# Kernel tuning notes

Hardware: AMD Instinct MI355X
Metric: run time of the kernel (lower is better)

## Reference

```python
import jax, jax.numpy as jnp
import numpy as np

B, IN_CH, D, H, W = 2, 4, 8, 224, 224
DS = 4
DIM, HEADS, HEAD_DIM, LAYERS = 256, 8, 32, 4
INNER = HEADS * HEAD_DIM
MLP = 4 * DIM
WS = (4, 8, 8)
SHIFT = (2, 4, 4)
WVOL = WS[0] * WS[1] * WS[2]
Hp, Wp = H // DS, W // DS
NW = (D // WS[0]) * (Hp // WS[1]) * (Wp // WS[2])
NBIAS = (2 * WS[0] - 1) * (2 * WS[1] - 1) * (2 * WS[2] - 1)


def _rel_index():
    c = np.stack(np.meshgrid(np.arange(WS[0]), np.arange(WS[1]), np.arange(WS[2]), indexing='ij')).reshape(3, -1)
    r = (c[:, :, None] - c[:, None, :]).transpose(1, 2, 0)
    r[..., 0] += WS[0] - 1
    r[..., 1] += WS[1] - 1
    r[..., 2] += WS[2] - 1
    return r[..., 0] * (2 * WS[1] - 1) * (2 * WS[2] - 1) + r[..., 1] * (2 * WS[2] - 1) + r[..., 2]

REL_IDX = jnp.asarray(_rel_index())  # (WVOL, WVOL)


def _shift_mask():
    # standard Swin shifted-window attention mask on the post-merge grid
    img = np.zeros((D, Hp, Wp), np.int32)
    cnt = 0
    sl = lambda w, s: (slice(0, -w), slice(-w, -s), slice(-s, None))
    for sd in sl(WS[0], SHIFT[0]):
        for sh in sl(WS[1], SHIFT[1]):
            for sw in sl(WS[2], SHIFT[2]):
                img[sd, sh, sw] = cnt
                cnt += 1
    m = img.reshape(D // WS[0], WS[0], Hp // WS[1], WS[1], Wp // WS[2], WS[2])
    m = m.transpose(0, 2, 4, 1, 3, 5).reshape(NW, WVOL)
    return jnp.asarray(np.where(m[:, None, :] != m[:, :, None], -1e9, 0.0).astype(np.float32))

ATTN_MASK = _shift_mask()  # (NW, WVOL, WVOL)


def layer_norm(x, s, b):
    mu = x.mean(-1, keepdims=True)
    var = x.var(-1, keepdims=True)
    return (x - mu) / jnp.sqrt(var + 1e-5) * s + b


def window_attention(x, qkv_w, out_w, out_b, bias_tab, shifted):
    # x: (B, D, Hp, Wp, C) channel-last
    if shifted:
        x = jnp.roll(x, (-SHIFT[0], -SHIFT[1], -SHIFT[2]), axis=(1, 2, 3))
    xw = x.reshape(B, D // WS[0], WS[0], Hp // WS[1], WS[1], Wp // WS[2], WS[2], DIM)
    xw = xw.transpose(0, 1, 3, 5, 2, 4, 6, 7).reshape(B, NW, WVOL, DIM)
    qkv = xw @ qkv_w  # (B, NW, WVOL, 3*INNER)
    q, k, v = jnp.split(qkv, 3, axis=-1)
    split = lambda t: t.reshape(B, NW, WVOL, HEADS, HEAD_DIM).transpose(0, 1, 3, 2, 4)
    q = split(q) * (HEAD_DIM ** -0.5)
    k, v = split(k), split(v)
    attn = jnp.einsum('bwhid,bwhjd->bwhij', q, k)  # (B, NW, H, WVOL, WVOL)
    bias = bias_tab[REL_IDX].transpose(2, 0, 1)  # (H, WVOL, WVOL)
    attn = attn + bias
    if shifted:
        attn = attn + ATTN_MASK[None, :, None]
    attn = jax.nn.softmax(attn, axis=-1)
    o = jnp.einsum('bwhij,bwhjd->bwhid', attn, v)
    o = o.transpose(0, 1, 3, 2, 4).reshape(B, NW, WVOL, INNER)
    o = o @ out_w + out_b
    o = o.reshape(B, D // WS[0], Hp // WS[1], Wp // WS[2], WS[0], WS[1], WS[2], DIM)
    o = o.transpose(0, 1, 4, 2, 5, 3, 6, 7).reshape(B, D, Hp, Wp, DIM)
    if shifted:
        o = jnp.roll(o, SHIFT, axis=(1, 2, 3))
    return o


def setup_inputs() -> dict:
    key = jax.random.key(0)
    ks = jax.random.split(key, 12)
    s = 0.02
    return {
        'x': jax.random.normal(ks[0], (B, IN_CH, D, H, W), jnp.float32),
        'conv_w': jax.random.normal(ks[1], (DIM, IN_CH, 1, DS, DS), jnp.float32) * s,
        'conv_b': jnp.zeros((DIM,), jnp.float32),
        'ln1_s': jnp.ones((LAYERS, DIM), jnp.float32),
        'ln1_b': jnp.zeros((LAYERS, DIM), jnp.float32),
        'qkv_w': jax.random.normal(ks[2], (LAYERS, DIM, 3 * INNER), jnp.float32) * s,
        'out_w': jax.random.normal(ks[3], (LAYERS, INNER, DIM), jnp.float32) * s,
        'out_b': jnp.zeros((LAYERS, DIM), jnp.float32),
        'bias_tab': jax.random.normal(ks[4], (LAYERS, NBIAS, HEADS), jnp.float32) * s,
        'ln2_s': jnp.ones((LAYERS, DIM), jnp.float32),
        'ln2_b': jnp.zeros((LAYERS, DIM), jnp.float32),
        'fc1_w': jax.random.normal(ks[5], (LAYERS, DIM, MLP), jnp.float32) * s,
        'fc1_b': jnp.zeros((LAYERS, MLP), jnp.float32),
        'fc2_w': jax.random.normal(ks[6], (LAYERS, MLP, DIM), jnp.float32) * s,
        'fc2_b': jnp.zeros((LAYERS, DIM), jnp.float32),
    }


def reference(x, conv_w, conv_b, ln1_s, ln1_b, qkv_w, out_w, out_b, bias_tab, ln2_s, ln2_b, fc1_w, fc1_b, fc2_w, fc2_b):
    # patch merge: Conv3d kernel (1, DS, DS) stride (1, DS, DS)
    y = jax.lax.conv_general_dilated(
        x, conv_w, window_strides=(1, DS, DS), padding='VALID',
        dimension_numbers=('NCDHW', 'OIDHW', 'NCDHW'))
    y = y + conv_b[None, :, None, None, None]
    y = y.transpose(0, 2, 3, 4, 1)  # (B, D, Hp, Wp, DIM) channel-last
    for i in range(LAYERS):
        shifted = (i % 2 == 1)
        y = y + window_attention(layer_norm(y, ln1_s[i], ln1_b[i]),
                                 qkv_w[i], out_w[i], out_b[i], bias_tab[i], shifted)
        h = layer_norm(y, ln2_s[i], ln2_b[i])
        h = jax.nn.gelu(h @ fc1_w[i] + fc1_b[i]) @ fc2_w[i] + fc2_b[i]
        y = y + h
    return y.transpose(0, 4, 1, 2, 3)  # (B, DIM, D, Hp, Wp)
```

## Files before the change

kernel.cpp:

```cpp
#include <hip/hip_runtime.h>

typedef unsigned short ushort_t;
typedef unsigned int   uint_t;

#define NTOK 50176
#define NWIN 98
#define NBIAS 1575

typedef __attribute__((ext_vector_type(8))) short bf16x8;
typedef __attribute__((ext_vector_type(4))) float floatx4;

static __device__ __forceinline__ ushort_t f2b(float f) {
    union { float f; uint_t u; } v; v.f = f;
    uint_t u = v.u + 0x7fffu + ((v.u >> 16) & 1u);
    return (ushort_t)(u >> 16);
}

__global__ void transpose_w(const float* __restrict__ src, ushort_t* __restrict__ dst,
                            int K, int N) {
    long base = (long)blockIdx.y * K * N;
    int idx = blockIdx.x * 256 + threadIdx.x;
    if (idx < K * N) {
        int k = idx / N, n = idx - k * N;
        dst[base + (long)n * K + k] = f2b(src[base + idx]);
    }
}

__global__ void cast_bf16(const float* __restrict__ src, ushort_t* __restrict__ dst, int n) {
    int i = blockIdx.x * 256 + threadIdx.x;
    if (i < n) dst[i] = f2b(src[i]);
}

__global__ void gen_btab(const float* __restrict__ bias_tab, float* __restrict__ Btab) {
    int slot = blockIdx.y;
    int layer, cls;
    if (slot == 0)      { layer = 0; cls = 0; }
    else if (slot < 9)  { layer = 1; cls = slot - 1; }
    else if (slot == 9) { layer = 2; cls = 0; }
    else                { layer = 3; cls = slot - 10; }
    int idx = blockIdx.x * 256 + threadIdx.x;
    int hd = idx >> 16;
    int ij = idx & 65535;
    int i = ij >> 8, j = ij & 255;
    int di = i >> 6, hi = (i >> 3) & 7, wi = i & 7;
    int dj = j >> 6, hj = (j >> 3) & 7, wj = j & 7;
    int rel = (di - dj + 3) * 225 + (hi - hj + 7) * 15 + (wi - wj + 7);
    float v = bias_tab[((long)layer * NBIAS + rel) * 8 + hd];
    int cd = cls >> 2, ch = (cls >> 1) & 1, cw = cls & 1;
    int ri = (cd ? (di < 2 ? 1 : 2) : 0) * 9 + (ch ? (hi < 4 ? 1 : 2) : 0) * 3 + (cw ? (wi < 4 ? 1 : 2) : 0);
    int rj = (cd ? (dj < 2 ? 1 : 2) : 0) * 9 + (ch ? (hj < 4 ? 1 : 2) : 0) * 3 + (cw ? (wj < 4 ? 1 : 2) : 0);
    if (ri != rj) v = -1e9f;
    Btab[(long)slot * 524288 + idx] = v * 1.4426950408889634f;
}

__global__ void im2row(const float* __restrict__ X, ushort_t* __restrict__ A) {
    int idx = blockIdx.x * 256 + threadIdx.x;
    int t = idx >> 4;
    int k = idx & 15;
    int ic = k >> 2, kh = k & 3;
    int w = t % 56, h = (t / 56) % 56, d = (t / 3136) % 8, b = t / 25088;
    long xi = (((long)(b * 4 + ic) * 8 + d) * 224 + (h * 4 + kh)) * 224 + w * 4;
    float4 u = *(const float4*)(X + xi);
    ushort_t* ap = A + (long)t * 64 + ic * 16 + kh * 4;
    ap[0] = f2b(u.x); ap[1] = f2b(u.y); ap[2] = f2b(u.z); ap[3] = f2b(u.w);
}

__global__ void ln_kernel(const float* __restrict__ Y, ushort_t* __restrict__ Xn,
                          const float* __restrict__ S, const float* __restrict__ Bb) {
    int wv = threadIdx.x >> 6, lane = threadIdx.x & 63;
    long t = (long)blockIdx.x * 4 + wv;
    const float* y = Y + t * 256;
    float v[4], s = 0.f, s2 = 0.f;
#pragma unroll
    for (int r = 0; r < 4; ++r) { v[r] = y[lane + 64 * r]; s += v[r]; s2 += v[r] * v[r]; }
#pragma unroll
    for (int off = 32; off; off >>= 1) { s += __shfl_xor(s, off, 64); s2 += __shfl_xor(s2, off, 64); }
    float mu = s * (1.f / 256.f);
    float var = s2 * (1.f / 256.f) - mu * mu;
    float rstd = rsqrtf(var + 1e-5f);
#pragma unroll
    for (int r = 0; r < 4; ++r) {
        int c = lane + 64 * r;
        Xn[t * 256 + c] = f2b((v[r] - mu) * rstd * S[c] + Bb[c]);
    }
}

__global__ __launch_bounds__(256, 2) void gemm_bt(
    const ushort_t* __restrict__ A, const ushort_t* __restrict__ BT,
    int M, int N, int K,
    const float* __restrict__ bias, int mode,
    ushort_t* __restrict__ C, float* __restrict__ Y) {
    __shared__ ushort_t As[128 * 32];
    __shared__ ushort_t Bs[128 * 32];
    const int tid = threadIdx.x;
    const int wv = tid >> 6;
    const int lane = tid & 63;
    const int quad = lane >> 4;
    const int l15 = lane & 15;
    const long m0 = (long)blockIdx.x * 128;
    const long n0 = (long)blockIdx.y * 128;
    const int wm = (wv & 1) * 64;
    const int wn = (wv >> 1) * 64;
    const int r_loc = lane >> 2;
    const int k_loc = (lane & 3) * 8;

    floatx4 acc[4][4] = {};

    const ushort_t* Ab = A + m0 * K;
    const ushort_t* Bb = BT + n0 * K;

    for (int kt = 0; kt < K; kt += 32) {
#pragma unroll
        for (int q = 0; q < 2; ++q) {
            int slot = wv * 2 + q;
            int row = slot * 16 + r_loc;
            __builtin_amdgcn_global_load_lds(
                (const __attribute__((address_space(1))) void*)(Ab + (long)row * K + kt + k_loc),
                (__attribute__((address_space(3))) void*)(As + slot * 512), 16, 0, 0);
            __builtin_amdgcn_global_load_lds(
                (const __attribute__((address_space(1))) void*)(Bb + (long)row * K + kt + k_loc),
                (__attribute__((address_space(3))) void*)(Bs + slot * 512), 16, 0, 0);
        }
        __syncthreads();
        bf16x8 af[4], bfr[4];
#pragma unroll
        for (int i = 0; i < 4; ++i) {
            af[i]  = *(const bf16x8*)(As + (wm + i * 16 + l15) * 32 + quad * 8);
            bfr[i] = *(const bf16x8*)(Bs + (wn + i * 16 + l15) * 32 + quad * 8);
        }
#pragma unroll
        for (int mi = 0; mi < 4; ++mi)
#pragma unroll
            for (int ni = 0; ni < 4; ++ni)
                acc[mi][ni] = __builtin_amdgcn_mfma_f32_16x16x32_bf16(af[mi], bfr[ni], acc[mi][ni], 0, 0, 0);
        __syncthreads();
    }

    if (mode == 2) {
#pragma unroll
        for (int mi = 0; mi < 4; ++mi)
#pragma unroll
            for (int ni = 0; ni < 4; ++ni) {
                long col = n0 + wn + ni * 16 + l15;
                float bv = bias[col];
#pragma unroll
                for (int r = 0; r < 4; ++r) {
                    long row = m0 + wm + mi * 16 + quad * 4 + r;
                    Y[row * N + col] += acc[mi][ni][r] + bv;
                }
            }
    } else if (mode == 3) {
#pragma unroll
        for (int mi = 0; mi < 4; ++mi)
#pragma unroll
            for (int ni = 0; ni < 4; ++ni) {
                long col = n0 + wn + ni * 16 + l15;
                float bv = bias[col];
#pragma unroll
                for (int r = 0; r < 4; ++r) {
                    long row = m0 + wm + mi * 16 + quad * 4 + r;
                    Y[row * N + col] = acc[mi][ni][r] + bv;
                }
            }
    } else {
#pragma unroll
        for (int mi = 0; mi < 4; ++mi)
#pragma unroll
            for (int ni = 0; ni < 4; ++ni) {
                long col = n0 + wn + ni * 16 + l15;
                float bv = bias ? bias[col] : 0.f;
#pragma unroll
                for (int r = 0; r < 4; ++r) {
                    long row = m0 + wm + mi * 16 + quad * 4 + r;
                    float v = acc[mi][ni][r] + bv;
                    if (mode == 1) {
                        float x3 = v * v * v;
                        v = 0.5f * v * (1.f + tanhf(0.7978845608028654f * (v + 0.044715f * x3)));
                    }
                    C[row * N + col] = f2b(v);
                }
            }
    }
}

#define PSTR 134
#define VTSTR 266
__global__ __launch_bounds__(512, 4) void attn_mfma(
    const ushort_t* __restrict__ QKV, ushort_t* __restrict__ O,
    const float* __restrict__ Btab, int shifted) {
    __shared__ ushort_t Ks[256 * 32];
    __shared__ ushort_t Vt[32 * VTSTR];
    __shared__ ushort_t Pl[8 * 16 * PSTR];
    __shared__ int tok_s[256];

    const int tid = threadIdx.x;
    const int wv = tid >> 6;
    const int lane = tid & 63;
    const int quad = lane >> 4;
    const int l15 = lane & 15;
    const int wdx = blockIdx.x, hd = blockIdx.y, b = blockIdx.z;
    const int wd = wdx / 49;
    const int wh = (wdx / 7) % 7;
    const int ww = wdx % 7;

    const int cls = shifted ? ((wd << 2) | ((wh == 6) << 1) | (ww == 6)) : 0;
    const float* bt = Btab + ((long)(cls * 8 + hd)) * 65536;

    if (tid < 256) {
        const int t = tid;
        const int di = t >> 6, hi = (t >> 3) & 7, wi = t & 7;
        const int d = wd * 4 + di, h = wh * 8 + hi, w = ww * 8 + wi;
        int d0 = d, h0 = h, w0 = w;
        if (shifted) { d0 = (d + 2) & 7; h0 = (h + 4) % 56; w0 = (w + 4) % 56; }
        const long tok = ((long)((b * 8 + d0) * 56 + h0)) * 56 + w0;
        tok_s[t] = (int)tok;
        const uint4* kp = (const uint4*)(QKV + tok * 768 + 256 + hd * 32);
        const uint4* vp = (const uint4*)(QKV + tok * 768 + 512 + hd * 32);
        uint4* kd = (uint4*)(Ks + t * 32);
#pragma unroll
        for (int p = 0; p < 4; ++p) kd[p] = kp[p];
#pragma unroll
        for (int p = 0; p < 4; ++p) {
            uint4 vvu = vp[p];
            uint_t uu[4] = {vvu.x, vvu.y, vvu.z, vvu.w};
#pragma unroll
            for (int e = 0; e < 4; ++e) {
                int dd = p * 8 + e * 2;
                Vt[dd * VTSTR + t]       = (ushort_t)(uu[e] & 0xffffu);
                Vt[(dd + 1) * VTSTR + t] = (ushort_t)(uu[e] >> 16);
            }
        }
    }
    __syncthreads();

    const float scale = 0.17677669529663687f * 1.4426950408889634f;
    ushort_t* Pw = Pl + wv * 16 * PSTR;

    for (int rg = 0; rg < 2; ++rg) {
        const int rti = wv * 2 + rg;
        bf16x8 aq;
        {
            int tq = tok_s[rti * 16 + l15];
            const uint4* qp = (const uint4*)(QKV + (long)tq * 768 + hd * 32 + quad * 8);
            union { uint4 u; bf16x8 v; } cv; cv.u = *qp; aq = cv.v;
        }
        const float* bp = bt + (long)(rti * 16 + quad * 4) * 256 + l15;
        floatx4 Sc[16];
        float m4[4] = {-3e38f, -3e38f, -3e38f, -3e38f};
#pragma unroll
        for (int hf = 0; hf < 2; ++hf) {
            float bb[8][4];
#pragma unroll
            for (int n8 = 0; n8 < 8; ++n8)
#pragma unroll
                for (int r = 0; r < 4; ++r)
                    bb[n8][r] = bp[r * 256 + (hf * 8 + n8) * 16];
#pragma unroll
            for (int n8 = 0; n8 < 8; ++n8) {
                const int nt = hf * 8 + n8;
                bf16x8 bk = *(const bf16x8*)(Ks + (nt * 16 + l15) * 32 + quad * 8);
                floatx4 z = {};
                Sc[nt] = __builtin_amdgcn_mfma_f32_16x16x32_bf16(aq, bk, z, 0, 0, 0);
            }
#pragma unroll
            for (int n8 = 0; n8 < 8; ++n8) {
                const int nt = hf * 8 + n8;
#pragma unroll
                for (int r = 0; r < 4; ++r) {
                    float s = fmaf(Sc[nt][r], scale, bb[n8][r]);
                    Sc[nt][r] = s;
                    m4[r] = fmaxf(m4[r], s);
                }
            }
        }
#pragma unroll
        for (int r = 0; r < 4; ++r) {
            m4[r] = fmaxf(m4[r], __shfl_xor(m4[r], 1));
            m4[r] = fmaxf(m4[r], __shfl_xor(m4[r], 2));
            m4[r] = fmaxf(m4[r], __shfl_xor(m4[r], 4));
            m4[r] = fmaxf(m4[r], __shfl_xor(m4[r], 8));
        }
        float l4[4] = {0.f, 0.f, 0.f, 0.f};
#pragma unroll
        for (int nt = 0; nt < 16; ++nt)
#pragma unroll
            for (int r = 0; r < 4; ++r) {
                float p = __builtin_amdgcn_exp2f(Sc[nt][r] - m4[r]);
                l4[r] += p;
                Sc[nt][r] = p;
            }
#pragma unroll
        for (int r = 0; r < 4; ++r) {
            l4[r] += __shfl_xor(l4[r], 1);
            l4[r] += __shfl_xor(l4[r], 2);
            l4[r] += __shfl_xor(l4[r], 4);
            l4[r] += __shfl_xor(l4[r], 8);
        }
        float inv4[4];
#pragma unroll
        for (int r = 0; r < 4; ++r) inv4[r] = 1.f / l4[r];

        floatx4 oa[2] = {};
#pragma unroll
        for (int hf = 0; hf < 2; ++hf) {
#pragma unroll
            for (int n8 = 0; n8 < 8; ++n8)
#pragma unroll
                for (int r = 0; r < 4; ++r)
                    Pw[(quad * 4 + r) * PSTR + n8 * 16 + l15] = f2b(Sc[hf * 8 + n8][r]);
            __builtin_amdgcn_s_waitcnt(0xC07F);
            __builtin_amdgcn_wave_barrier();
#pragma unroll
            for (int ct = 0; ct < 2; ++ct)
#pragma unroll
                for (int kt = 0; kt < 4; ++kt) {
                    bf16x8 ap = *(const bf16x8*)(Pw + l15 * PSTR + kt * 32 + quad * 8);
                    bf16x8 bv = *(const bf16x8*)(Vt + (ct * 16 + l15) * VTSTR + hf * 128 + kt * 32 + quad * 8);
                    oa[ct] = __builtin_amdgcn_mfma_f32_16x16x32_bf16(ap, bv, oa[ct], 0, 0, 0);
                }
            __builtin_amdgcn_s_waitcnt(0xC07F);
            __builtin_amdgcn_wave_barrier();
        }
#pragma unroll
        for (int ct = 0; ct < 2; ++ct)
#pragma unroll
            for (int r = 0; r < 4; ++r) {
                int i = rti * 16 + quad * 4 + r;
                long tq = tok_s[i];
                O[tq * 256 + hd * 32 + ct * 16 + l15] = f2b(oa[ct][r] * inv4[r]);
            }
    }
}

__global__ void out_permute(const float* __restrict__ Y, float* __restrict__ Out) {
    __shared__ float tile[64][65];
    const int t0 = blockIdx.x * 64;
    const int c0 = blockIdx.y * 64;
    const int tid = threadIdx.x;
    const int a = tid >> 6;
    const int bx = tid & 63;
#pragma unroll
    for (int s8 = 0; s8 < 16; ++s8) {
        int tt = a + s8 * 4;
        tile[tt][bx] = Y[(long)(t0 + tt) * 256 + c0 + bx];
    }
    __syncthreads();
#pragma unroll
    for (int s8 = 0; s8 < 16; ++s8) {
        int cc = a + s8 * 4;
        int tok = t0 + bx;
        int bb = tok / 25088;
        int rem = tok - bb * 25088;
        Out[((long)(bb * 256 + c0 + cc)) * 25088 + rem] = tile[bx][cc];
    }
}

extern "C" void kernel_launch(void* const* d_in, const int* in_sizes, int n_in,
                              void* d_out, int out_size, void* d_ws, size_t ws_size,
                              hipStream_t stream) {
    (void)in_sizes; (void)n_in; (void)out_size; (void)ws_size;
    const float* x        = (const float*)d_in[0];
    const float* conv_w   = (const float*)d_in[1];
    const float* conv_b   = (const float*)d_in[2];
    const float* ln1_s    = (const float*)d_in[3];
    const float* ln1_b    = (const float*)d_in[4];
    const float* qkv_w    = (const float*)d_in[5];
    const float* out_w    = (const float*)d_in[6];
    const float* out_b    = (const float*)d_in[7];
    const float* bias_tab = (const float*)d_in[8];
    const float* ln2_s    = (const float*)d_in[9];
    const float* ln2_b    = (const float*)d_in[10];
    const float* fc1_w    = (const float*)d_in[11];
    const float* fc1_b    = (const float*)d_in[12];
    const float* fc2_w    = (const float*)d_in[13];
    const float* fc2_b    = (const float*)d_in[14];
    float* out = (float*)d_out;

    char* ws = (char*)d_ws;
    float*    y    = (float*)ws;    ws += (size_t)NTOK * 256 * 4;
    ushort_t* big  = (ushort_t*)ws; ws += (size_t)NTOK * 1024 * 2;
    ushort_t* xob  = (ushort_t*)ws; ws += (size_t)NTOK * 256 * 2;
    ushort_t* bt_qkv = (ushort_t*)ws; ws += (size_t)4 * 768 * 256 * 2;
    ushort_t* bt_out = (ushort_t*)ws; ws += (size_t)4 * 256 * 256 * 2;
    ushort_t* bt_fc1 = (ushort_t*)ws; ws += (size_t)4 * 1024 * 256 * 2;
    ushort_t* bt_fc2 = (ushort_t*)ws; ws += (size_t)4 * 256 * 1024 * 2;
    ushort_t* cw_bf  = (ushort_t*)ws; ws += (size_t)256 * 64 * 2;
    float*    btab   = (float*)ws;  ws += (size_t)18 * 524288 * 4;

    transpose_w<<<dim3((256 * 768 + 255) / 256, 4), 256, 0, stream>>>(qkv_w, bt_qkv, 256, 768);
    transpose_w<<<dim3((256 * 256 + 255) / 256, 4), 256, 0, stream>>>(out_w, bt_out, 256, 256);
    transpose_w<<<dim3((256 * 1024 + 255) / 256, 4), 256, 0, stream>>>(fc1_w, bt_fc1, 256, 1024);
    transpose_w<<<dim3((1024 * 256 + 255) / 256, 4), 256, 0, stream>>>(fc2_w, bt_fc2, 1024, 256);
    gen_btab<<<dim3(2048, 18), 256, 0, stream>>>(bias_tab, btab);

    cast_bf16<<<(256 * 64 + 255) / 256, 256, 0, stream>>>(conv_w, cw_bf, 256 * 64);
    im2row<<<NTOK * 16 / 256, 256, 0, stream>>>(x, big);
    gemm_bt<<<dim3(NTOK / 128, 2), 256, 0, stream>>>(
        big, cw_bf, NTOK, 256, 64, conv_b, 3, nullptr, y);

    static const int base_slot[4] = {0, 1, 9, 10};
    for (int i = 0; i < 4; ++i) {
        int sh = i & 1;
        ln_kernel<<<NTOK / 4, 256, 0, stream>>>(y, xob, ln1_s + i * 256, ln1_b + i * 256);
        gemm_bt<<<dim3(NTOK / 128, 6), 256, 0, stream>>>(
            xob, bt_qkv + (size_t)i * 768 * 256, NTOK, 768, 256, nullptr, 0, big, nullptr);
        attn_mfma<<<dim3(NWIN, 8, 2), 512, 0, stream>>>(
            big, xob, btab + (size_t)base_slot[i] * 524288, sh);
        gemm_bt<<<dim3(NTOK / 128, 2), 256, 0, stream>>>(
            xob, bt_out + (size_t)i * 256 * 256, NTOK, 256, 256, out_b + i * 256, 2, nullptr, y);
        ln_kernel<<<NTOK / 4, 256, 0, stream>>>(y, xob, ln2_s + i * 256, ln2_b + i * 256);
        gemm_bt<<<dim3(NTOK / 128, 8), 256, 0, stream>>>(
            xob, bt_fc1 + (size_t)i * 1024 * 256, NTOK, 1024, 256, fc1_b + i * 1024, 1, big, nullptr);
        gemm_bt<<<dim3(NTOK / 128, 2), 256, 0, stream>>>(
            big, bt_fc2 + (size_t)i * 256 * 1024, NTOK, 256, 1024, fc2_b + i * 256, 2, nullptr, y);
    }

    out_permute<<<dim3(NTOK / 64, 4), 256, 0, stream>>>(y, out);
}
```

Measured before the change: 1.400 ms.

## Double-buffer GEMM LDS tiles, vectorize layernorm, use exp-based GELU

The GEMM kernel now uses two LDS buffers and prefetches the next K-tile while computing on the current one, cutting one barrier per iteration and overlapping global loads with MFMA work. Layernorm loads and stores are vectorized with float4/ushort4 accesses. The tanh-based GELU is rewritten as x*sigmoid(2u) using hardware exp2 and reciprocal intrinsics. LDS use per GEMM block doubles, and the fast intrinsics give slightly lower accuracy.

Measured after the change: 1.358 ms. -3.0%, faster.

```diff
diff --git a/kernel.cpp b/kernel.cpp
--- a/kernel.cpp
+++ b/kernel.cpp
@@ -9,6 +9,7 @@
 
 typedef __attribute__((ext_vector_type(8))) short bf16x8;
 typedef __attribute__((ext_vector_type(4))) float floatx4;
+typedef __attribute__((ext_vector_type(4))) ushort_t ushortx4;
 
 static __device__ __forceinline__ ushort_t f2b(float f) {
     union { float f; uint_t u; } v; v.f = f;
@@ -69,20 +70,22 @@
                           const float* __restrict__ S, const float* __restrict__ Bb) {
     int wv = threadIdx.x >> 6, lane = threadIdx.x & 63;
     long t = (long)blockIdx.x * 4 + wv;
-    const float* y = Y + t * 256;
-    float v[4], s = 0.f, s2 = 0.f;
-#pragma unroll
-    for (int r = 0; r < 4; ++r) { v[r] = y[lane + 64 * r]; s += v[r]; s2 += v[r] * v[r]; }
+    float4 u = *(const float4*)(Y + t * 256 + lane * 4);
+    float s = u.x + u.y + u.z + u.w;
+    float s2 = u.x * u.x + u.y * u.y + u.z * u.z + u.w * u.w;
 #pragma unroll
     for (int off = 32; off; off >>= 1) { s += __shfl_xor(s, off, 64); s2 += __shfl_xor(s2, off, 64); }
     float mu = s * (1.f / 256.f);
     float var = s2 * (1.f / 256.f) - mu * mu;
     float rstd = rsqrtf(var + 1e-5f);
-#pragma unroll
-    for (int r = 0; r < 4; ++r) {
-        int c = lane + 64 * r;
-        Xn[t * 256 + c] = f2b((v[r] - mu) * rstd * S[c] + Bb[c]);
-    }
+    float4 sc = *(const float4*)(S + lane * 4);
+    float4 bb = *(const float4*)(Bb + lane * 4);
+    ushortx4 o;
+    o.x = f2b((u.x - mu) * rstd * sc.x + bb.x);
+    o.y = f2b((u.y - mu) * rstd * sc.y + bb.y);
+    o.z = f2b((u.z - mu) * rstd * sc.z + bb.z);
+    o.w = f2b((u.w - mu) * rstd * sc.w + bb.w);
+    *(ushortx4*)(Xn + t * 256 + lane * 4) = o;
 }
 
 __global__ __launch_bounds__(256, 2) void gemm_bt(
@@ -90,8 +93,8 @@
     int M, int N, int K,
     const float* __restrict__ bias, int mode,
     ushort_t* __restrict__ C, float* __restrict__ Y) {
-    __shared__ ushort_t As[128 * 32];
-    __shared__ ushort_t Bs[128 * 32];
+    __shared__ ushort_t As[2][128 * 32];
+    __shared__ ushort_t Bs[2][128 * 32];
     const int tid = threadIdx.x;
     const int wv = tid >> 6;
     const int lane = tid & 63;
@@ -108,25 +111,40 @@
 
     const ushort_t* Ab = A + m0 * K;
     const ushort_t* Bb = BT + n0 * K;
-
-    for (int kt = 0; kt < K; kt += 32) {
-#pragma unroll
-        for (int q = 0; q < 2; ++q) {
-            int slot = wv * 2 + q;
-            int row = slot * 16 + r_loc;
-            __builtin_amdgcn_global_load_lds(
-                (const __attribute__((address_space(1))) void*)(Ab + (long)row * K + kt + k_loc),
-                (__attribute__((address_space(3))) void*)(As + slot * 512), 16, 0, 0);
-            __builtin_amdgcn_global_load_lds(
-                (const __attribute__((address_space(1))) void*)(Bb + (long)row * K + kt + k_loc),
-                (__attribute__((address_space(3))) void*)(Bs + slot * 512), 16, 0, 0);
-        }
-        __syncthreads();
+    const int slot = wv * 2;
+    const int row0 = slot * 16 + r_loc;
+    const int nkt = K >> 5;
+
+#pragma unroll
+    for (int q = 0; q < 2; ++q) {
+        __builtin_amdgcn_global_load_lds(
+            (const __attribute__((address_space(1))) void*)(Ab + (long)(row0 + q * 16) * K + k_loc),
+            (__attribute__((address_space(3))) void*)(&As[0][(slot + q) * 512]), 16, 0, 0);
+        __builtin_amdgcn_global_load_lds(
+            (const __attribute__((address_space(1))) void*)(Bb + (long)(row0 + q * 16) * K + k_loc),
+            (__attribute__((address_space(3))) void*)(&Bs[0][(slot + q) * 512]), 16, 0, 0);
+    }
+    __syncthreads();
+
+    int cur = 0;
+    for (int t = 0; t < nkt; ++t) {
+        if (t + 1 < nkt) {
+            const int kt = (t + 1) << 5;
+#pragma unroll
+            for (int q = 0; q < 2; ++q) {
+                __builtin_amdgcn_global_load_lds(
+                    (const __attribute__((address_space(1))) void*)(Ab + (long)(row0 + q * 16) * K + kt + k_loc),
+                    (__attribute__((address_space(3))) void*)(&As[cur ^ 1][(slot + q) * 512]), 16, 0, 0);
+                __builtin_amdgcn_global_load_lds(
+                    (const __attribute__((address_space(1))) void*)(Bb + (long)(row0 + q * 16) * K + kt + k_loc),
+                    (__attribute__((address_space(3))) void*)(&Bs[cur ^ 1][(slot + q) * 512]), 16, 0, 0);
+            }
+        }
         bf16x8 af[4], bfr[4];
 #pragma unroll
         for (int i = 0; i < 4; ++i) {
-            af[i]  = *(const bf16x8*)(As + (wm + i * 16 + l15) * 32 + quad * 8);
-            bfr[i] = *(const bf16x8*)(Bs + (wn + i * 16 + l15) * 32 + quad * 8);
+            af[i]  = *(const bf16x8*)(&As[cur][(wm + i * 16 + l15) * 32 + quad * 8]);
+            bfr[i] = *(const bf16x8*)(&Bs[cur][(wn + i * 16 + l15) * 32 + quad * 8]);
         }
 #pragma unroll
         for (int mi = 0; mi < 4; ++mi)
@@ -134,6 +152,7 @@
             for (int ni = 0; ni < 4; ++ni)
                 acc[mi][ni] = __builtin_amdgcn_mfma_f32_16x16x32_bf16(af[mi], bfr[ni], acc[mi][ni], 0, 0, 0);
         __syncthreads();
+        cur ^= 1;
     }
 
     if (mode == 2) {
@@ -174,8 +193,9 @@
                     long row = m0 + wm + mi * 16 + quad * 4 + r;
                     float v = acc[mi][ni][r] + bv;
                     if (mode == 1) {
-                        float x3 = v * v * v;
-                        v = 0.5f * v * (1.f + tanhf(0.7978845608028654f * (v + 0.044715f * x3)));
+                        float u = 0.7978845608028654f * (v + 0.044715f * v * v * v);
+                        float e = __builtin_amdgcn_exp2f(-2.8853900817779268f * u);
+                        v = v * __builtin_amdgcn_rcpf(1.f + e);
                     }
                     C[row * N + col] = f2b(v);
                 }
```
